# Kernel tuning notes

Hardware: AMD Instinct MI355X
Metric: run time of the kernel (lower is better)

The kernel has to match this reference:

```python
import jax, jax.numpy as jnp
import numpy as np

DT = 0.02      # integration step (module default)
ORDER = 5      # Taylor-series order (module default)
B = 2_000_000  # batch of independent Lorenz states


def setup_inputs() -> dict:
    key = jax.random.key(0)
    x = jax.random.normal(key, (B, 3), dtype=jnp.float32)
    return {"x": x}


def _build_A(x):
    # State-dependent Lorenz Jacobian, batched: [B, 3, 3]
    x1 = x[:, 0]
    z = jnp.zeros_like(x1)
    c = lambda v: jnp.full_like(x1, v)
    row0 = jnp.stack([c(-10.0), c(10.0), z], axis=-1)
    row1 = jnp.stack([c(28.0), c(-1.0), -x1], axis=-1)
    row2 = jnp.stack([z, x1, c(-8.0 / 3.0)], axis=-1)
    return jnp.stack([row0, row1, row2], axis=1)


def reference(x):
    # F = sum_{j=0}^{ORDER} (A*dt)^j / j!   (Taylor matrix exponential), then F @ x
    A_dt = _build_A(x) * DT                                   # [B,3,3]
    I = jnp.broadcast_to(jnp.eye(3, dtype=x.dtype), A_dt.shape)
    F = I
    term = I
    for j in range(1, ORDER + 1):
        term = jnp.einsum('bij,bjk->bik', term, A_dt) / j     # term = A_dt^j / j!
        F = F + term
    return jnp.einsum('bij,bj->bi', F, x)                     # [B,3]
```

## Files before the change

kernel.cpp:

```cpp
#include <hip/hip_runtime.h>

#define LORENZ_DT 0.02f

__device__ __forceinline__ void lorenz_one(float x0, float x1, float x2,
                                           float& o0, float& o1, float& o2) {
    const float a00 = -10.0f * LORENZ_DT;
    const float a01 =  10.0f * LORENZ_DT;
    const float a10 =  28.0f * LORENZ_DT;
    const float a11 =  -1.0f * LORENZ_DT;
    const float a22 = (-8.0f / 3.0f) * LORENZ_DT;
    const float a12 = -x0 * LORENZ_DT;
    const float a21 =  x0 * LORENZ_DT;

    float t00 = 1.f, t01 = 0.f, t02 = 0.f;
    float t10 = 0.f, t11 = 1.f, t12 = 0.f;
    float t20 = 0.f, t21 = 0.f, t22 = 1.f;
    float F00 = 1.f, F01 = 0.f, F02 = 0.f;
    float F10 = 0.f, F11 = 1.f, F12 = 0.f;
    float F20 = 0.f, F21 = 0.f, F22 = 1.f;

#pragma unroll
    for (int j = 1; j <= 5; ++j) {
        const float inv = 1.0f / (float)j;
        float n00 = (t00 * a00 + t01 * a10) * inv;
        float n01 = (t00 * a01 + t01 * a11 + t02 * a21) * inv;
        float n02 = (t01 * a12 + t02 * a22) * inv;
        float n10 = (t10 * a00 + t11 * a10) * inv;
        float n11 = (t10 * a01 + t11 * a11 + t12 * a21) * inv;
        float n12 = (t11 * a12 + t12 * a22) * inv;
        float n20 = (t20 * a00 + t21 * a10) * inv;
        float n21 = (t20 * a01 + t21 * a11 + t22 * a21) * inv;
        float n22 = (t21 * a12 + t22 * a22) * inv;
        t00 = n00; t01 = n01; t02 = n02;
        t10 = n10; t11 = n11; t12 = n12;
        t20 = n20; t21 = n21; t22 = n22;
        F00 += t00; F01 += t01; F02 += t02;
        F10 += t10; F11 += t11; F12 += t12;
        F20 += t20; F21 += t21; F22 += t22;
    }

    o0 = F00 * x0 + F01 * x1 + F02 * x2;
    o1 = F10 * x0 + F11 * x1 + F12 * x2;
    o2 = F20 * x0 + F21 * x1 + F22 * x2;
}

__global__ __launch_bounds__(256) void lorenz_kernel(const float* __restrict__ x,
                                                     float* __restrict__ out, int n) {
    const int g = blockIdx.x * blockDim.x + threadIdx.x;
    const int base = g * 4;
    if (base >= n) return;

    if (base + 4 <= n) {
        const float4* xv = (const float4*)x;
        float4* ov = (float4*)out;
        float4 va = xv[g * 3 + 0];
        float4 vb = xv[g * 3 + 1];
        float4 vc = xv[g * 3 + 2];
        float xs[12] = {va.x, va.y, va.z, va.w,
                        vb.x, vb.y, vb.z, vb.w,
                        vc.x, vc.y, vc.z, vc.w};
        float os[12];
#pragma unroll
        for (int e = 0; e < 4; ++e) {
            lorenz_one(xs[e * 3 + 0], xs[e * 3 + 1], xs[e * 3 + 2],
                       os[e * 3 + 0], os[e * 3 + 1], os[e * 3 + 2]);
        }
        ov[g * 3 + 0] = make_float4(os[0], os[1], os[2], os[3]);
        ov[g * 3 + 1] = make_float4(os[4], os[5], os[6], os[7]);
        ov[g * 3 + 2] = make_float4(os[8], os[9], os[10], os[11]);
    } else {
        for (int e = base; e < n; ++e) {
            float x0 = x[e * 3 + 0], x1 = x[e * 3 + 1], x2 = x[e * 3 + 2];
            float o0, o1, o2;
            lorenz_one(x0, x1, x2, o0, o1, o2);
            out[e * 3 + 0] = o0;
            out[e * 3 + 1] = o1;
            out[e * 3 + 2] = o2;
        }
    }
}

extern "C" void kernel_launch(void* const* d_in, const int* in_sizes, int n_in,
                              void* d_out, int out_size, void* d_ws, size_t ws_size,
                              hipStream_t stream) {
    const float* x = (const float*)d_in[0];
    float* out = (float*)d_out;
    const int n = in_sizes[0] / 3;
    const int groups = (n + 3) / 4;
    const int block = 256;
    const int grid = (groups + block - 1) / block;
    lorenz_kernel<<<grid, block, 0, stream>>>(x, out, n);
}
```

Baseline: 77.47 us.

## Stage loads and stores through padded LDS for fully coalesced float4 access

Each block now loads its contiguous chunk with fully coalesced float4 nontemporal loads into padded shared memory, each thread reads its 12 floats from LDS, computes, writes them back to LDS, and the block stores coalesced float4 with nontemporal stores. The goal is better DRAM access patterns than the per-thread stride-3 float4 accesses, plus bypassing cache for streaming data. It adds two barriers and LDS traffic, with padding to limit bank conflicts.

```diff
diff --git a/kernel.cpp b/kernel.cpp
--- a/kernel.cpp
+++ b/kernel.cpp
@@ -1,6 +1,8 @@
 #include <hip/hip_runtime.h>
 
 #define LORENZ_DT 0.02f
+
+typedef float vfloat4 __attribute__((ext_vector_type(4)));
 
 __device__ __forceinline__ void lorenz_one(float x0, float x1, float x2,
                                            float& o0, float& o1, float& o2) {
@@ -44,38 +46,87 @@
     o2 = F20 * x0 + F21 * x1 + F22 * x2;
 }
 
+
+#define BLOCK 256
+#define EPT 4
+#define ELEMS_PER_BLOCK (BLOCK * EPT)
+#define F4_PER_BLOCK (ELEMS_PER_BLOCK * 3 / 4)
+#define F4_PADDED (F4_PER_BLOCK + F4_PER_BLOCK / 24)
+
+__device__ __forceinline__ int pad4(int i) { return i + i / 24; }
+
 __global__ __launch_bounds__(256) void lorenz_kernel(const float* __restrict__ x,
                                                      float* __restrict__ out, int n) {
-    const int g = blockIdx.x * blockDim.x + threadIdx.x;
-    const int base = g * 4;
-    if (base >= n) return;
+    const int tid = threadIdx.x;
+    const int blockElemBase = blockIdx.x * ELEMS_PER_BLOCK;
 
-    if (base + 4 <= n) {
-        const float4* xv = (const float4*)x;
-        float4* ov = (float4*)out;
-        float4 va = xv[g * 3 + 0];
-        float4 vb = xv[g * 3 + 1];
-        float4 vc = xv[g * 3 + 2];
-        float xs[12] = {va.x, va.y, va.z, va.w,
-                        vb.x, vb.y, vb.z, vb.w,
-                        vc.x, vc.y, vc.z, vc.w};
-        float os[12];
+    __shared__ vfloat4 lbuf[F4_PADDED];
+    float* lfs = (float*)lbuf;
+
+    if (blockElemBase + ELEMS_PER_BLOCK <= n) {
+        const vfloat4* x4 = (const vfloat4*)x;
+        vfloat4* o4 = (vfloat4*)out;
+        const size_t b4 = (size_t)blockIdx.x * F4_PER_BLOCK;
+
+#pragma unroll
+        for (int j = 0; j < 3; ++j) {
+            vfloat4 v = __builtin_nontemporal_load(&x4[b4 + tid + BLOCK * j]);
+            lbuf[pad4(tid + BLOCK * j)] = v;
+        }
+        __syncthreads();
+
+        const int wb = 12 * tid + 4 * (tid >> 3);
+        float xs[12], os[12];
+#pragma unroll
+        for (int k = 0; k < 12; ++k) xs[k] = lfs[wb + k];
+
 #pragma unroll
         for (int e = 0; e < 4; ++e) {
             lorenz_one(xs[e * 3 + 0], xs[e * 3 + 1], xs[e * 3 + 2],
                        os[e * 3 + 0], os[e * 3 + 1], os[e * 3 + 2]);
         }
-        ov[g * 3 + 0] = make_float4(os[0], os[1], os[2], os[3]);
-        ov[g * 3 + 1] = make_float4(os[4], os[5], os[6], os[7]);
-        ov[g * 3 + 2] = make_float4(os[8], os[9], os[10], os[11]);
+
+#pragma unroll
+        for (int k = 0; k < 12; ++k) lfs[wb + k] = os[k];
+        __syncthreads();
+
+#pragma unroll
+        for (int j = 0; j < 3; ++j) {
+            vfloat4 v = lbuf[pad4(tid + BLOCK * j)];
+            __builtin_nontemporal_store(v, &o4[b4 + tid + BLOCK * j]);
+        }
     } else {
-        for (int e = base; e < n; ++e) {
-            float x0 = x[e * 3 + 0], x1 = x[e * 3 + 1], x2 = x[e * 3 + 2];
-            float o0, o1, o2;
-            lorenz_one(x0, x1, x2, o0, o1, o2);
-            out[e * 3 + 0] = o0;
-            out[e * 3 + 1] = o1;
-            out[e * 3 + 2] = o2;
+        const int g = blockElemBase / EPT + tid;
+        const int base = g * 4;
+        if (base >= n) return;
+
+        if (base + 4 <= n) {
+            const float4* xv = (const float4*)x;
+            float4* ov = (float4*)out;
+            float4 va = xv[g * 3 + 0];
+            float4 vb = xv[g * 3 + 1];
+            float4 vc = xv[g * 3 + 2];
+            float xs[12] = {va.x, va.y, va.z, va.w,
+                            vb.x, vb.y, vb.z, vb.w,
+                            vc.x, vc.y, vc.z, vc.w};
+            float os[12];
+#pragma unroll
+            for (int e = 0; e < 4; ++e) {
+                lorenz_one(xs[e * 3 + 0], xs[e * 3 + 1], xs[e * 3 + 2],
+                           os[e * 3 + 0], os[e * 3 + 1], os[e * 3 + 2]);
+            }
+            ov[g * 3 + 0] = make_float4(os[0], os[1], os[2], os[3]);
+            ov[g * 3 + 1] = make_float4(os[4], os[5], os[6], os[7]);
+            ov[g * 3 + 2] = make_float4(os[8], os[9], os[10], os[11]);
+        } else {
+            for (int e = base; e < n; ++e) {
+                float x0 = x[e * 3 + 0], x1 = x[e * 3 + 1], x2 = x[e * 3 + 2];
+                float o0, o1, o2;
+                lorenz_one(x0, x1, x2, o0, o1, o2);
+                out[e * 3 + 0] = o0;
+                out[e * 3 + 1] = o1;
+                out[e * 3 + 2] = o2;
+            }
         }
     }
 }
@@ -86,8 +137,6 @@
     const float* x = (const float*)d_in[0];
     float* out = (float*)d_out;
     const int n = in_sizes[0] / 3;
-    const int groups = (n + 3) / 4;
-    const int block = 256;
-    const int grid = (groups + block - 1) / block;
-    lorenz_kernel<<<grid, block, 0, stream>>>(x, out, n);
+    const int grid = (n + ELEMS_PER_BLOCK - 1) / ELEMS_PER_BLOCK;
+    lorenz_kernel<<<grid, BLOCK, 0, stream>>>(x, out, n);
 }
```

Result: no change. 78.92 us (+1.9%).
